# Optimization experiments

Hardware: AMD Instinct MI355X
Metric: run time of the kernel (lower is better)

The kernel has to match this reference:

```python
import jax, jax.numpy as jnp
import numpy as np

B, S, E, H = 4, 2048, 1024, 16
D = E // H  # head dim = 64

def setup_inputs() -> dict:
    key = jax.random.key(0)
    k1, k2, k3 = jax.random.split(key, 3)
    scale = 0.02
    return {
        "x": jax.random.normal(k1, (B, S, E), dtype=jnp.float32),
        "W_qkv": jax.random.normal(k2, (E, 3 * E), dtype=jnp.float32) * scale,
        "b_qkv": jnp.zeros((3 * E,), dtype=jnp.float32),
        "W_o": jax.random.normal(k3, (E, E), dtype=jnp.float32) * scale,
        "b_o": jnp.zeros((E,), dtype=jnp.float32),
    }

def reference(x, W_qkv, b_qkv, W_o, b_o):
    # dropout is identity in eval mode
    qkv = x @ W_qkv + b_qkv                      # [B, S, 3E]
    q, k, v = jnp.split(qkv, 3, axis=-1)          # each [B, S, E]
    def split_heads(t):
        return t.reshape(B, S, H, D).transpose(0, 2, 1, 3)  # [B, H, S, D]
    q, k, v = split_heads(q), split_heads(k), split_heads(v)
    scores = jnp.einsum("bhsd,bhtd->bhst", q, k) / jnp.sqrt(jnp.float32(D))
    causal = jnp.tril(jnp.ones((S, S), dtype=bool))
    scores = jnp.where(causal[None, None], scores, jnp.float32(-jnp.inf))
    attn = jax.nn.softmax(scores, axis=-1)        # [B, H, S, S]
    out = jnp.einsum("bhst,bhtd->bhsd", attn, v)  # [B, H, S, D]
    out = out.transpose(0, 2, 1, 3).reshape(B, S, E)
    return out @ W_o + b_o
```

## Files before the change

### kernel.cpp

```cpp
#include <hip/hip_runtime.h>
#include <stdint.h>

typedef __bf16 bf16_t;
typedef __bf16 bf16x8 __attribute__((ext_vector_type(8)));
typedef float f32x4 __attribute__((ext_vector_type(4)));

#define LOG2E 1.44269504088896340736f

__device__ __forceinline__ float fexp2(float x) {
#if __has_builtin(__builtin_amdgcn_exp2f)
    return __builtin_amdgcn_exp2f(x);
#else
    return exp2f(x);
#endif
}

__device__ __forceinline__ void gld_lds16(const bf16_t* g, bf16_t* l) {
    __builtin_amdgcn_global_load_lds(
        (__attribute__((address_space(1))) void*)(bf16_t*)g,
        (__attribute__((address_space(3))) void*)l,
        16, 0, 0);
}

__global__ __launch_bounds__(256) void prep_k(
    const float* __restrict__ x, bf16_t* __restrict__ xb,
    const float* __restrict__ Wqkv, bf16_t* __restrict__ wqkvT,
    const float* __restrict__ Wo, bf16_t* __restrict__ woT)
{
    __shared__ float t[32][33];
    const int tid = threadIdx.x;
    int blk = blockIdx.x;
    if (blk < 8192) {
        int i = blk * 1024 + tid * 4;
        float4 v = *(const float4*)(x + i);
        union { bf16_t b[4]; uint2 u; } u;
        u.b[0] = (bf16_t)v.x; u.b[1] = (bf16_t)v.y; u.b[2] = (bf16_t)v.z; u.b[3] = (bf16_t)v.w;
        *(uint2*)(xb + i) = u.u;
        return;
    }
    const float* in; bf16_t* out; int C, bx, by;
    if (blk < 11264) { blk -= 8192; in = Wqkv; out = wqkvT; C = 3072; bx = blk % 96; by = blk / 96; }
    else             { blk -= 11264; in = Wo;   out = woT;   C = 1024; bx = blk % 32; by = blk / 32; }
    const int R = 1024;
    const int tx = tid & 31, ty = tid >> 5;
    const int c0 = bx * 32, r0 = by * 32;
    #pragma unroll
    for (int j = 0; j < 32; j += 8)
        t[ty + j][tx] = in[(size_t)(r0 + ty + j) * C + c0 + tx];
    __syncthreads();
    #pragma unroll
    for (int j = 0; j < 32; j += 8)
        out[(size_t)(c0 + ty + j) * R + r0 + tx] = (bf16_t)t[tx][ty + j];
}

__device__ __forceinline__ void gemm_body_pipe(
    const bf16_t* __restrict__ A, const bf16_t* __restrict__ Bt,
    bf16_t* Al, bf16_t* Bl, f32x4 (&acc)[4][4], int m0, int n0)
{
    const int tid = threadIdx.x;
    const int w = tid >> 6, lane = tid & 63;
    const int l15 = lane & 15, quad = lane >> 4;
    const int wm = w >> 2, wn = w & 3;

    const int srow = lane >> 3;
    const int scg = ((lane & 7) ^ srow) * 8;
    const bf16_t* Ag = A  + (size_t)(m0 + w * 16 + srow) * 1024 + scg;
    const bf16_t* Bg = Bt + (size_t)(n0 + w * 32 + srow) * 1024 + scg;

    const int rc0 = (quad ^ (l15 & 7)) * 8;
    const int rc1 = ((quad + 4) ^ (l15 & 7)) * 8;

    auto stage0 = [&](int kt, int ss) {
        gld_lds16(Ag + kt * 64,                       Al + ss * 8192  + (w * 16) * 64);
        gld_lds16(Ag + kt * 64 + (size_t)8 * 1024,    Al + ss * 8192  + (w * 16 + 8) * 64);
        gld_lds16(Bg + kt * 64,                       Bl + ss * 16384 + (w * 32) * 64);
    };
    auto stage1 = [&](int kt, int ss) {
        gld_lds16(Bg + kt * 64 + (size_t)8 * 1024,    Bl + ss * 16384 + (w * 32 + 8) * 64);
        gld_lds16(Bg + kt * 64 + (size_t)16 * 1024,   Bl + ss * 16384 + (w * 32 + 16) * 64);
        gld_lds16(Bg + kt * 64 + (size_t)24 * 1024,   Bl + ss * 16384 + (w * 32 + 24) * 64);
    };

    stage0(0, 0); stage1(0, 0);
    stage0(1, 1); stage1(1, 1);
    asm volatile("s_waitcnt vmcnt(6)" ::: "memory");
    __builtin_amdgcn_s_barrier();

    int cs = 0, ss = 2;
    for (int t = 0; t < 16; ++t) {
        const bf16_t* Ab = Al + cs * 8192;
        const bf16_t* Bb = Bl + cs * 16384;

        {
            bf16x8 af[4], bfr[4];
            #pragma unroll
            for (int mi = 0; mi < 4; mi++)
                af[mi] = *(const bf16x8*)(Ab + (wm * 64 + mi * 16 + l15) * 64 + rc0);
            #pragma unroll
            for (int ni = 0; ni < 4; ni++)
                bfr[ni] = *(const bf16x8*)(Bb + (wn * 64 + ni * 16 + l15) * 64 + rc0);
            if (t < 14) stage0(t + 2, ss);
            __builtin_amdgcn_s_barrier();
            __builtin_amdgcn_s_setprio(1);
            #pragma unroll
            for (int mi = 0; mi < 4; mi++)
                #pragma unroll
                for (int ni = 0; ni < 4; ni++)
                    acc[mi][ni] = __builtin_amdgcn_mfma_f32_16x16x32_bf16(
                        af[mi], bfr[ni], acc[mi][ni], 0, 0, 0);
            __builtin_amdgcn_s_setprio(0);
            __builtin_amdgcn_s_barrier();
        }

        {
            bf16x8 af[4], bfr[4];
            #pragma unroll
            for (int mi = 0; mi < 4; mi++)
                af[mi] = *(const bf16x8*)(Ab + (wm * 64 + mi * 16 + l15) * 64 + rc1);
            #pragma unroll
            for (int ni = 0; ni < 4; ni++)
                bfr[ni] = *(const bf16x8*)(Bb + (wn * 64 + ni * 16 + l15) * 64 + rc1);
            if (t < 14) {
                stage1(t + 2, ss);
                asm volatile("s_waitcnt vmcnt(6)" ::: "memory");
            } else if (t == 14) {
                asm volatile("s_waitcnt vmcnt(0)" ::: "memory");
            }
            __builtin_amdgcn_s_barrier();
            __builtin_amdgcn_s_setprio(1);
            #pragma unroll
            for (int mi = 0; mi < 4; mi++)
                #pragma unroll
                for (int ni = 0; ni < 4; ni++)
                    acc[mi][ni] = __builtin_amdgcn_mfma_f32_16x16x32_bf16(
                        af[mi], bfr[ni], acc[mi][ni], 0, 0, 0);
            __builtin_amdgcn_s_setprio(0);
            __builtin_amdgcn_s_barrier();
        }

        cs = (cs == 2) ? 0 : cs + 1;
        ss = (ss == 2) ? 0 : ss + 1;
    }
}

__global__ __launch_bounds__(512) void gemm_qkv_k(
    const bf16_t* __restrict__ X, const bf16_t* __restrict__ WT,
    const float* __restrict__ bias,
    bf16_t* __restrict__ Qb, bf16_t* __restrict__ Kb, bf16_t* __restrict__ VTb)
{
    __shared__ bf16_t Al[3 * 128 * 64];
    __shared__ bf16_t Bl[3 * 256 * 64];
    const int tid = threadIdx.x;
    const int lane = tid & 63, w = tid >> 6;
    const int l15 = lane & 15, quad = lane >> 4;
    const int wm = w >> 2, wn = w & 3;
    const int n0 = blockIdx.x * 256;
    const int m0 = blockIdx.y * 128;

    f32x4 acc[4][4];
    #pragma unroll
    for (int mi = 0; mi < 4; mi++)
        #pragma unroll
        for (int ni = 0; ni < 4; ni++) acc[mi][ni] = (f32x4){0.f, 0.f, 0.f, 0.f};

    gemm_body_pipe(WT, X, Al, Bl, acc, m0, n0);

    const float QSCALE = 0.125f * LOG2E;
    const int region = m0 >> 10;
    #pragma unroll
    for (int mi = 0; mi < 4; mi++) {
        const int mbase = m0 + wm * 64 + mi * 16 + quad * 4;
        const float4 bia = *(const float4*)(bias + mbase);
        const float ba[4] = {bia.x, bia.y, bia.z, bia.w};
        const int col = mbase & 1023;
        const int h = col >> 6, dbase = col & 63;
        #pragma unroll
        for (int ni = 0; ni < 4; ni++) {
            const int n = n0 + wn * 64 + ni * 16 + l15;
            const int b = n >> 11, s = n & 2047;
            if (region == 0) {
                union { bf16_t bv[4]; uint2 u; } u;
                #pragma unroll
                for (int r = 0; r < 4; r++)
                    u.bv[r] = (bf16_t)((acc[mi][ni][r] + ba[r]) * QSCALE);
                *(uint2*)(Qb + (((size_t)b * 16 + h) * 2048 + s) * 64 + dbase) = u.u;
            } else if (region == 1) {
                union { bf16_t bv[4]; uint2 u; } u;
                #pragma unroll
                for (int r = 0; r < 4; r++)
                    u.bv[r] = (bf16_t)(acc[mi][ni][r] + ba[r]);
                *(uint2*)(Kb + (((size_t)b * 16 + h) * 2048 + s) * 64 + dbase) = u.u;
            } else {
                bf16_t* dst = VTb + (((size_t)b * 16 + h) * 64 + dbase) * 2048 + s;
                #pragma unroll
                for (int r = 0; r < 4; r++)
                    dst[(size_t)r * 2048] = (bf16_t)(acc[mi][ni][r] + ba[r]);
            }
        }
    }
}

__global__ __launch_bounds__(256) void attn_k(
    const bf16_t* __restrict__ Qb, const bf16_t* __restrict__ Kb,
    const bf16_t* __restrict__ VTb, bf16_t* __restrict__ Ob)
{
    __shared__ bf16_t Kl[64 * 64];
    __shared__ bf16_t Vl[64 * 64];
    __shared__ bf16_t Pl[4][16 * 72];

    const int tid = threadIdx.x;
    const int w = tid >> 6, lane = tid & 63;
    const int l15 = lane & 15, quad = lane >> 4;
    const int idx = blockIdx.x;
    const int qt = 31 - (idx >> 6);
    const int bh = idx & 63;
    const int b = bh >> 4, h = bh & 15;
    const int q0 = qt * 64;

    const bf16_t* Qp = Qb + (size_t)bh * 2048 * 64;
    const bf16_t* Kp = Kb + (size_t)bh * 2048 * 64;
    const bf16_t* Vp = VTb + (size_t)bh * 64 * 2048;

    const int srow = w * 16 + (lane >> 3);
    const int scol = ((lane & 7) ^ ((lane >> 3) & 7)) * 8;
    const int rc0 = (quad ^ (l15 & 7)) * 8;
    const int rc1 = ((quad + 4) ^ (l15 & 7)) * 8;

    const int qrow = q0 + w * 16 + l15;
    bf16x8 aq0 = *(const bf16x8*)(Qp + (size_t)qrow * 64 + quad * 8);
    bf16x8 aq1 = *(const bf16x8*)(Qp + (size_t)qrow * 64 + 32 + quad * 8);

    bf16x8 vone;
    #pragma unroll
    for (int j = 0; j < 8; j++) vone[j] = (bf16_t)1.0f;

    f32x4 o[4];
    #pragma unroll
    for (int ni = 0; ni < 4; ni++) o[ni] = (f32x4){0.f, 0.f, 0.f, 0.f};
    f32x4 lacc = (f32x4){0.f, 0.f, 0.f, 0.f};
    const int qloc = w * 16 + l15;

    for (int kv0 = 0; kv0 <= q0; kv0 += 64) {
        __syncthreads();
        gld_lds16(Kp + (size_t)(kv0 + srow) * 64 + scol, Kl + (w * 16) * 64);
        gld_lds16(Kp + (size_t)(kv0 + srow + 8) * 64 + scol, Kl + (w * 16 + 8) * 64);
        gld_lds16(Vp + (size_t)srow * 2048 + kv0 + scol, Vl + (w * 16) * 64);
        gld_lds16(Vp + (size_t)(srow + 8) * 2048 + kv0 + scol, Vl + (w * 16 + 8) * 64);
        __syncthreads();

        f32x4 sv[4];
        #pragma unroll
        for (int ni = 0; ni < 4; ni++) {
            bf16x8 ak0 = *(const bf16x8*)(Kl + (ni * 16 + l15) * 64 + rc0);
            bf16x8 ak1 = *(const bf16x8*)(Kl + (ni * 16 + l15) * 64 + rc1);
            f32x4 z = (f32x4){0.f, 0.f, 0.f, 0.f};
            z = __builtin_amdgcn_mfma_f32_16x16x32_bf16(ak0, aq0, z, 0, 0, 0);
            z = __builtin_amdgcn_mfma_f32_16x16x32_bf16(ak1, aq1, z, 0, 0, 0);
            sv[ni] = z;
        }

        if (kv0 == q0) {
            #pragma unroll
            for (int ni = 0; ni < 4; ni++)
                #pragma unroll
                for (int r = 0; r < 4; r++)
                    if (ni * 16 + quad * 4 + r > qloc) sv[ni][r] = -INFINITY;
        }

        #pragma unroll
        for (int ni = 0; ni < 4; ni++) {
            union { bf16_t bv[4]; uint2 u; } pk;
            #pragma unroll
            for (int r = 0; r < 4; r++) pk.bv[r] = (bf16_t)fexp2(sv[ni][r]);
            *(uint2*)(&Pl[w][l15 * 72 + ni * 16 + quad * 4]) = pk.u;
        }

        bf16x8 pa0 = *(const bf16x8*)(&Pl[w][l15 * 72 + quad * 8]);
        bf16x8 pa1 = *(const bf16x8*)(&Pl[w][l15 * 72 + 32 + quad * 8]);
        #pragma unroll
        for (int ni = 0; ni < 4; ni++) {
            bf16x8 bv0 = *(const bf16x8*)(Vl + (ni * 16 + l15) * 64 + rc0);
            bf16x8 bv1 = *(const bf16x8*)(Vl + (ni * 16 + l15) * 64 + rc1);
            o[ni] = __builtin_amdgcn_mfma_f32_16x16x32_bf16(bv0, pa0, o[ni], 0, 0, 0);
            o[ni] = __builtin_amdgcn_mfma_f32_16x16x32_bf16(bv1, pa1, o[ni], 0, 0, 0);
        }
        lacc = __builtin_amdgcn_mfma_f32_16x16x32_bf16(vone, pa0, lacc, 0, 0, 0);
        lacc = __builtin_amdgcn_mfma_f32_16x16x32_bf16(vone, pa1, lacc, 0, 0, 0);
    }

    const float inv = 1.0f / lacc[0];
    const int s = q0 + w * 16 + l15;
    bf16_t* obase = Ob + ((size_t)b * 2048 + s) * 1024 + h * 64;
    #pragma unroll
    for (int ni = 0; ni < 4; ni++) {
        union { bf16_t bv[4]; uint2 u; } u;
        #pragma unroll
        for (int r = 0; r < 4; r++) u.bv[r] = (bf16_t)(o[ni][r] * inv);
        *(uint2*)(obase + ni * 16 + quad * 4) = u.u;
    }
}

__global__ __launch_bounds__(512) void gemm_out_k(
    const bf16_t* __restrict__ O, const bf16_t* __restrict__ WT,
    const float* __restrict__ bias, float* __restrict__ out)
{
    __shared__ bf16_t Al[3 * 128 * 64];
    __shared__ bf16_t Bl[3 * 256 * 64];
    const int tid = threadIdx.x;
    const int lane = tid & 63, w = tid >> 6;
    const int l15 = lane & 15, quad = lane >> 4;
    const int wm = w >> 2, wn = w & 3;
    const int n0 = blockIdx.x * 256;
    const int m0 = blockIdx.y * 128;

    f32x4 acc[4][4];
    #pragma unroll
    for (int mi = 0; mi < 4; mi++)
        #pragma unroll
        for (int ni = 0; ni < 4; ni++) acc[mi][ni] = (f32x4){0.f, 0.f, 0.f, 0.f};

    gemm_body_pipe(WT, O, Al, Bl, acc, m0, n0);

    #pragma unroll
    for (int mi = 0; mi < 4; mi++) {
        const int mbase = m0 + wm * 64 + mi * 16 + quad * 4;
        const float4 bia = *(const float4*)(bias + mbase);
        #pragma unroll
        for (int ni = 0; ni < 4; ni++) {
            const int n = n0 + wn * 64 + ni * 16 + l15;
            float4 v;
            v.x = acc[mi][ni][0] + bia.x;
            v.y = acc[mi][ni][1] + bia.y;
            v.z = acc[mi][ni][2] + bia.z;
            v.w = acc[mi][ni][3] + bia.w;
            *(float4*)(out + (size_t)n * 1024 + mbase) = v;
        }
    }
}


extern "C" void kernel_launch(void* const* d_in, const int* in_sizes, int n_in,
                              void* d_out, int out_size, void* d_ws, size_t ws_size,
                              hipStream_t stream) {
    const float* x     = (const float*)d_in[0];
    const float* W_qkv = (const float*)d_in[1];
    const float* b_qkv = (const float*)d_in[2];
    const float* W_o   = (const float*)d_in[3];
    const float* b_o   = (const float*)d_in[4];
    float* out = (float*)d_out;

    char* ws = (char*)d_ws;
    size_t off = 0;
    auto alloc = [&](size_t bytes) -> void* {
        void* p = ws + off;
        off += (bytes + 255) & ~(size_t)255;
        return p;
    };
    bf16_t* xb    = (bf16_t*)alloc((size_t)8192 * 1024 * 2);
    bf16_t* wqkvT = (bf16_t*)alloc((size_t)3072 * 1024 * 2);
    bf16_t* woT   = (bf16_t*)alloc((size_t)1024 * 1024 * 2);
    bf16_t* Qb    = (bf16_t*)alloc((size_t)8192 * 1024 * 2);
    bf16_t* Kb    = (bf16_t*)alloc((size_t)8192 * 1024 * 2);
    bf16_t* VTb   = (bf16_t*)alloc((size_t)8192 * 1024 * 2);
    bf16_t* Ob    = xb;

    prep_k<<<12288, 256, 0, stream>>>(x, xb, W_qkv, wqkvT, W_o, woT);
    gemm_qkv_k<<<dim3(32, 24), 512, 0, stream>>>(xb, wqkvT, b_qkv, Qb, Kb, VTb);
    attn_k<<<2048, 256, 0, stream>>>(Qb, Kb, VTb, Ob);
    gemm_out_k<<<dim3(32, 8), 512, 0, stream>>>(Ob, woT, b_o, out);
}
```

Baseline: 237.4 us.

## Rewrite QKV GEMM with 256x256 tiles and double-buffered four-phase MFMA schedule

The QKV projection GEMM now uses a standalone kernel with a 256x256 block tile (8 warps each computing 128x64), double-buffered LDS and a four-phase interleave of fragment loads, async global-to-LDS staging and MFMA bursts. The grid is halved to 32x12. The goal is more operand reuse per LDS byte and fewer blocks. The costs are more accumulator registers (launch bounds of 512 threads with 2 blocks per CU), a full vmcnt(0) wait each iteration instead of a deeper three-stage pipeline, and fewer blocks to fill the CUs. The attention kernel is moved in the file but its code is unchanged.

```diff
diff --git a/kernel.cpp b/kernel.cpp
--- a/kernel.cpp
+++ b/kernel.cpp
@@ -53,6 +53,271 @@
         out[(size_t)(c0 + ty + j) * R + r0 + tx] = (bf16_t)t[tx][ty + j];
 }
 
+__global__ __launch_bounds__(512, 2) void gemm_qkv_k(
+    const bf16_t* __restrict__ X, const bf16_t* __restrict__ WT,
+    const float* __restrict__ bias,
+    bf16_t* __restrict__ Qb, bf16_t* __restrict__ Kb, bf16_t* __restrict__ VTb)
+{
+    __shared__ bf16_t Al[2 * 256 * 64];
+    __shared__ bf16_t Bl[2 * 256 * 64];
+    const int tid = threadIdx.x;
+    const int lane = tid & 63, w = tid >> 6;
+    const int l15 = lane & 15, quad = lane >> 4;
+    const int wr = w >> 2, wc = w & 3;
+    const int n0 = blockIdx.x * 256;
+    const int m0 = blockIdx.y * 256;
+
+    const int srow = lane >> 3;
+    const int scg = ((lane & 7) ^ srow) * 8;
+    const bf16_t* Ag = WT + (size_t)(m0 + w * 32 + srow) * 1024 + scg;
+    const bf16_t* Bg = X  + (size_t)(n0 + w * 32 + srow) * 1024 + scg;
+
+    const int rc0 = (quad ^ (l15 & 7)) * 8;
+    const int rc1 = ((quad + 4) ^ (l15 & 7)) * 8;
+
+    f32x4 acc[8][4];
+    #pragma unroll
+    for (int mi = 0; mi < 8; mi++)
+        #pragma unroll
+        for (int ni = 0; ni < 4; ni++) acc[mi][ni] = (f32x4){0.f, 0.f, 0.f, 0.f};
+
+    auto stageA = [&](int kt, int t) {
+        #pragma unroll
+        for (int j = 0; j < 4; j++)
+            gld_lds16(Ag + (size_t)kt * 64 + (size_t)(j * 8) * 1024,
+                      Al + t * 16384 + (w * 32 + j * 8) * 64);
+    };
+    auto stageB = [&](int kt, int t) {
+        #pragma unroll
+        for (int j = 0; j < 4; j++)
+            gld_lds16(Bg + (size_t)kt * 64 + (size_t)(j * 8) * 1024,
+                      Bl + t * 16384 + (w * 32 + j * 8) * 64);
+    };
+
+    stageA(0, 0); stageB(0, 0);
+    asm volatile("s_waitcnt vmcnt(0)" ::: "memory");
+    __builtin_amdgcn_s_barrier();
+
+    int cs = 0;
+    #pragma unroll 1
+    for (int n = 0; n < 16; ++n) {
+        const bf16_t* Ab = Al + cs * 16384;
+        const bf16_t* Bb = Bl + cs * 16384;
+        bf16x8 afr[4][2], bfr[4][2];
+
+        #pragma unroll
+        for (int q = 0; q < 4; q++) {
+            afr[q][0] = *(const bf16x8*)(Ab + (wr * 128 + q * 16 + l15) * 64 + rc0);
+            afr[q][1] = *(const bf16x8*)(Ab + (wr * 128 + q * 16 + l15) * 64 + rc1);
+        }
+        #pragma unroll
+        for (int ni = 0; ni < 2; ni++) {
+            bfr[ni][0] = *(const bf16x8*)(Bb + (wc * 64 + ni * 16 + l15) * 64 + rc0);
+            bfr[ni][1] = *(const bf16x8*)(Bb + (wc * 64 + ni * 16 + l15) * 64 + rc1);
+        }
+        if (n < 15) stageA(n + 1, cs ^ 1);
+        __builtin_amdgcn_s_barrier();
+        __builtin_amdgcn_s_setprio(1);
+        #pragma unroll
+        for (int q = 0; q < 4; q++)
+            #pragma unroll
+            for (int ni = 0; ni < 2; ni++) {
+                acc[q][ni] = __builtin_amdgcn_mfma_f32_16x16x32_bf16(
+                    afr[q][0], bfr[ni][0], acc[q][ni], 0, 0, 0);
+                acc[q][ni] = __builtin_amdgcn_mfma_f32_16x16x32_bf16(
+                    afr[q][1], bfr[ni][1], acc[q][ni], 0, 0, 0);
+            }
+        __builtin_amdgcn_s_setprio(0);
+
+        #pragma unroll
+        for (int ni = 2; ni < 4; ni++) {
+            bfr[ni][0] = *(const bf16x8*)(Bb + (wc * 64 + ni * 16 + l15) * 64 + rc0);
+            bfr[ni][1] = *(const bf16x8*)(Bb + (wc * 64 + ni * 16 + l15) * 64 + rc1);
+        }
+        if (n < 15) stageB(n + 1, cs ^ 1);
+        __builtin_amdgcn_s_barrier();
+        __builtin_amdgcn_s_setprio(1);
+        #pragma unroll
+        for (int q = 0; q < 4; q++)
+            #pragma unroll
+            for (int ni = 2; ni < 4; ni++) {
+                acc[q][ni] = __builtin_amdgcn_mfma_f32_16x16x32_bf16(
+                    afr[q][0], bfr[ni][0], acc[q][ni], 0, 0, 0);
+                acc[q][ni] = __builtin_amdgcn_mfma_f32_16x16x32_bf16(
+                    afr[q][1], bfr[ni][1], acc[q][ni], 0, 0, 0);
+            }
+        __builtin_amdgcn_s_setprio(0);
+
+        #pragma unroll
+        for (int q = 0; q < 4; q++) {
+            afr[q][0] = *(const bf16x8*)(Ab + (wr * 128 + 64 + q * 16 + l15) * 64 + rc0);
+            afr[q][1] = *(const bf16x8*)(Ab + (wr * 128 + 64 + q * 16 + l15) * 64 + rc1);
+        }
+        __builtin_amdgcn_s_barrier();
+        __builtin_amdgcn_s_setprio(1);
+        #pragma unroll
+        for (int q = 0; q < 4; q++)
+            #pragma unroll
+            for (int ni = 2; ni < 4; ni++) {
+                acc[4 + q][ni] = __builtin_amdgcn_mfma_f32_16x16x32_bf16(
+                    afr[q][0], bfr[ni][0], acc[4 + q][ni], 0, 0, 0);
+                acc[4 + q][ni] = __builtin_amdgcn_mfma_f32_16x16x32_bf16(
+                    afr[q][1], bfr[ni][1], acc[4 + q][ni], 0, 0, 0);
+            }
+        __builtin_amdgcn_s_setprio(0);
+
+        asm volatile("s_waitcnt vmcnt(0)" ::: "memory");
+        __builtin_amdgcn_s_barrier();
+        __builtin_amdgcn_s_setprio(1);
+        #pragma unroll
+        for (int q = 0; q < 4; q++)
+            #pragma unroll
+            for (int ni = 0; ni < 2; ni++) {
+                acc[4 + q][ni] = __builtin_amdgcn_mfma_f32_16x16x32_bf16(
+                    afr[q][0], bfr[ni][0], acc[4 + q][ni], 0, 0, 0);
+                acc[4 + q][ni] = __builtin_amdgcn_mfma_f32_16x16x32_bf16(
+                    afr[q][1], bfr[ni][1], acc[4 + q][ni], 0, 0, 0);
+            }
+        __builtin_amdgcn_s_setprio(0);
+
+        cs ^= 1;
+    }
+
+    const float QSCALE = 0.125f * LOG2E;
+    const int region = m0 >> 10;
+    #pragma unroll
+    for (int mi = 0; mi < 8; mi++) {
+        const int mbase = m0 + wr * 128 + mi * 16 + quad * 4;
+        const float4 bia = *(const float4*)(bias + mbase);
+        const float ba[4] = {bia.x, bia.y, bia.z, bia.w};
+        const int col = mbase & 1023;
+        const int h = col >> 6, dbase = col & 63;
+        #pragma unroll
+        for (int ni = 0; ni < 4; ni++) {
+            const int n = n0 + wc * 64 + ni * 16 + l15;
+            const int b = n >> 11, s = n & 2047;
+            if (region == 0) {
+                union { bf16_t bv[4]; uint2 u; } u;
+                #pragma unroll
+                for (int r = 0; r < 4; r++)
+                    u.bv[r] = (bf16_t)((acc[mi][ni][r] + ba[r]) * QSCALE);
+                *(uint2*)(Qb + (((size_t)b * 16 + h) * 2048 + s) * 64 + dbase) = u.u;
+            } else if (region == 1) {
+                union { bf16_t bv[4]; uint2 u; } u;
+                #pragma unroll
+                for (int r = 0; r < 4; r++)
+                    u.bv[r] = (bf16_t)(acc[mi][ni][r] + ba[r]);
+                *(uint2*)(Kb + (((size_t)b * 16 + h) * 2048 + s) * 64 + dbase) = u.u;
+            } else {
+                bf16_t* dst = VTb + (((size_t)b * 16 + h) * 64 + dbase) * 2048 + s;
+                #pragma unroll
+                for (int r = 0; r < 4; r++)
+                    dst[(size_t)r * 2048] = (bf16_t)(acc[mi][ni][r] + ba[r]);
+            }
+        }
+    }
+}
+
+__global__ __launch_bounds__(256) void attn_k(
+    const bf16_t* __restrict__ Qb, const bf16_t* __restrict__ Kb,
+    const bf16_t* __restrict__ VTb, bf16_t* __restrict__ Ob)
+{
+    __shared__ bf16_t Kl[64 * 64];
+    __shared__ bf16_t Vl[64 * 64];
+    __shared__ bf16_t Pl[4][16 * 72];
+
+    const int tid = threadIdx.x;
+    const int w = tid >> 6, lane = tid & 63;
+    const int l15 = lane & 15, quad = lane >> 4;
+    const int idx = blockIdx.x;
+    const int qt = 31 - (idx >> 6);
+    const int bh = idx & 63;
+    const int b = bh >> 4, h = bh & 15;
+    const int q0 = qt * 64;
+
+    const bf16_t* Qp = Qb + (size_t)bh * 2048 * 64;
+    const bf16_t* Kp = Kb + (size_t)bh * 2048 * 64;
+    const bf16_t* Vp = VTb + (size_t)bh * 64 * 2048;
+
+    const int srow = w * 16 + (lane >> 3);
+    const int scol = ((lane & 7) ^ ((lane >> 3) & 7)) * 8;
+    const int rc0 = (quad ^ (l15 & 7)) * 8;
+    const int rc1 = ((quad + 4) ^ (l15 & 7)) * 8;
+
+    const int qrow = q0 + w * 16 + l15;
+    bf16x8 aq0 = *(const bf16x8*)(Qp + (size_t)qrow * 64 + quad * 8);
+    bf16x8 aq1 = *(const bf16x8*)(Qp + (size_t)qrow * 64 + 32 + quad * 8);
+
+    bf16x8 vone;
+    #pragma unroll
+    for (int j = 0; j < 8; j++) vone[j] = (bf16_t)1.0f;
+
+    f32x4 o[4];
+    #pragma unroll
+    for (int ni = 0; ni < 4; ni++) o[ni] = (f32x4){0.f, 0.f, 0.f, 0.f};
+    f32x4 lacc = (f32x4){0.f, 0.f, 0.f, 0.f};
+    const int qloc = w * 16 + l15;
+
+    for (int kv0 = 0; kv0 <= q0; kv0 += 64) {
+        __syncthreads();
+        gld_lds16(Kp + (size_t)(kv0 + srow) * 64 + scol, Kl + (w * 16) * 64);
+        gld_lds16(Kp + (size_t)(kv0 + srow + 8) * 64 + scol, Kl + (w * 16 + 8) * 64);
+        gld_lds16(Vp + (size_t)srow * 2048 + kv0 + scol, Vl + (w * 16) * 64);
+        gld_lds16(Vp + (size_t)(srow + 8) * 2048 + kv0 + scol, Vl + (w * 16 + 8) * 64);
+        __syncthreads();
+
+        f32x4 sv[4];
+        #pragma unroll
+        for (int ni = 0; ni < 4; ni++) {
+            bf16x8 ak0 = *(const bf16x8*)(Kl + (ni * 16 + l15) * 64 + rc0);
+            bf16x8 ak1 = *(const bf16x8*)(Kl + (ni * 16 + l15) * 64 + rc1);
+            f32x4 z = (f32x4){0.f, 0.f, 0.f, 0.f};
+            z = __builtin_amdgcn_mfma_f32_16x16x32_bf16(ak0, aq0, z, 0, 0, 0);
+            z = __builtin_amdgcn_mfma_f32_16x16x32_bf16(ak1, aq1, z, 0, 0, 0);
+            sv[ni] = z;
+        }
+
+        if (kv0 == q0) {
+            #pragma unroll
+            for (int ni = 0; ni < 4; ni++)
+                #pragma unroll
+                for (int r = 0; r < 4; r++)
+                    if (ni * 16 + quad * 4 + r > qloc) sv[ni][r] = -INFINITY;
+        }
+
+        #pragma unroll
+        for (int ni = 0; ni < 4; ni++) {
+            union { bf16_t bv[4]; uint2 u; } pk;
+            #pragma unroll
+            for (int r = 0; r < 4; r++) pk.bv[r] = (bf16_t)fexp2(sv[ni][r]);
+            *(uint2*)(&Pl[w][l15 * 72 + ni * 16 + quad * 4]) = pk.u;
+        }
+
+        bf16x8 pa0 = *(const bf16x8*)(&Pl[w][l15 * 72 + quad * 8]);
+        bf16x8 pa1 = *(const bf16x8*)(&Pl[w][l15 * 72 + 32 + quad * 8]);
+        #pragma unroll
+        for (int ni = 0; ni < 4; ni++) {
+            bf16x8 bv0 = *(const bf16x8*)(Vl + (ni * 16 + l15) * 64 + rc0);
+            bf16x8 bv1 = *(const bf16x8*)(Vl + (ni * 16 + l15) * 64 + rc1);
+            o[ni] = __builtin_amdgcn_mfma_f32_16x16x32_bf16(bv0, pa0, o[ni], 0, 0, 0);
+            o[ni] = __builtin_amdgcn_mfma_f32_16x16x32_bf16(bv1, pa1, o[ni], 0, 0, 0);
+        }
+        lacc = __builtin_amdgcn_mfma_f32_16x16x32_bf16(vone, pa0, lacc, 0, 0, 0);
+        lacc = __builtin_amdgcn_mfma_f32_16x16x32_bf16(vone, pa1, lacc, 0, 0, 0);
+    }
+
+    const float inv = 1.0f / lacc[0];
+    const int s = q0 + w * 16 + l15;
+    bf16_t* obase = Ob + ((size_t)b * 2048 + s) * 1024 + h * 64;
+    #pragma unroll
+    for (int ni = 0; ni < 4; ni++) {
+        union { bf16_t bv[4]; uint2 u; } u;
+        #pragma unroll
+        for (int r = 0; r < 4; r++) u.bv[r] = (bf16_t)(o[ni][r] * inv);
+        *(uint2*)(obase + ni * 16 + quad * 4) = u.u;
+    }
+}
+
 __device__ __forceinline__ void gemm_body_pipe(
     const bf16_t* __restrict__ A, const bf16_t* __restrict__ Bt,
     bf16_t* Al, bf16_t* Bl, f32x4 (&acc)[4][4], int m0, int n0)
@@ -90,7 +355,6 @@
     for (int t = 0; t < 16; ++t) {
         const bf16_t* Ab = Al + cs * 8192;
         const bf16_t* Bb = Bl + cs * 16384;
-
         {
             bf16x8 af[4], bfr[4];
             #pragma unroll
@@ -111,7 +375,6 @@
             __builtin_amdgcn_s_setprio(0);
             __builtin_amdgcn_s_barrier();
         }
-
         {
             bf16x8 af[4], bfr[4];
             #pragma unroll
@@ -137,166 +400,8 @@
             __builtin_amdgcn_s_setprio(0);
             __builtin_amdgcn_s_barrier();
         }
-
         cs = (cs == 2) ? 0 : cs + 1;
         ss = (ss == 2) ? 0 : ss + 1;
-    }
-}
-
-__global__ __launch_bounds__(512) void gemm_qkv_k(
-    const bf16_t* __restrict__ X, const bf16_t* __restrict__ WT,
-    const float* __restrict__ bias,
-    bf16_t* __restrict__ Qb, bf16_t* __restrict__ Kb, bf16_t* __restrict__ VTb)
-{
-    __shared__ bf16_t Al[3 * 128 * 64];
-    __shared__ bf16_t Bl[3 * 256 * 64];
-    const int tid = threadIdx.x;
-    const int lane = tid & 63, w = tid >> 6;
-    const int l15 = lane & 15, quad = lane >> 4;
-    const int wm = w >> 2, wn = w & 3;
-    const int n0 = blockIdx.x * 256;
-    const int m0 = blockIdx.y * 128;
-
-    f32x4 acc[4][4];
-    #pragma unroll
-    for (int mi = 0; mi < 4; mi++)
-        #pragma unroll
-        for (int ni = 0; ni < 4; ni++) acc[mi][ni] = (f32x4){0.f, 0.f, 0.f, 0.f};
-
-    gemm_body_pipe(WT, X, Al, Bl, acc, m0, n0);
-
-    const float QSCALE = 0.125f * LOG2E;
-    const int region = m0 >> 10;
-    #pragma unroll
-    for (int mi = 0; mi < 4; mi++) {
-        const int mbase = m0 + wm * 64 + mi * 16 + quad * 4;
-        const float4 bia = *(const float4*)(bias + mbase);
-        const float ba[4] = {bia.x, bia.y, bia.z, bia.w};
-        const int col = mbase & 1023;
-        const int h = col >> 6, dbase = col & 63;
-        #pragma unroll
-        for (int ni = 0; ni < 4; ni++) {
-            const int n = n0 + wn * 64 + ni * 16 + l15;
-            const int b = n >> 11, s = n & 2047;
-            if (region == 0) {
-                union { bf16_t bv[4]; uint2 u; } u;
-                #pragma unroll
-                for (int r = 0; r < 4; r++)
-                    u.bv[r] = (bf16_t)((acc[mi][ni][r] + ba[r]) * QSCALE);
-                *(uint2*)(Qb + (((size_t)b * 16 + h) * 2048 + s) * 64 + dbase) = u.u;
-            } else if (region == 1) {
-                union { bf16_t bv[4]; uint2 u; } u;
-                #pragma unroll
-                for (int r = 0; r < 4; r++)
-                    u.bv[r] = (bf16_t)(acc[mi][ni][r] + ba[r]);
-                *(uint2*)(Kb + (((size_t)b * 16 + h) * 2048 + s) * 64 + dbase) = u.u;
-            } else {
-                bf16_t* dst = VTb + (((size_t)b * 16 + h) * 64 + dbase) * 2048 + s;
-                #pragma unroll
-                for (int r = 0; r < 4; r++)
-                    dst[(size_t)r * 2048] = (bf16_t)(acc[mi][ni][r] + ba[r]);
-            }
-        }
-    }
-}
-
-__global__ __launch_bounds__(256) void attn_k(
-    const bf16_t* __restrict__ Qb, const bf16_t* __restrict__ Kb,
-    const bf16_t* __restrict__ VTb, bf16_t* __restrict__ Ob)
-{
-    __shared__ bf16_t Kl[64 * 64];
-    __shared__ bf16_t Vl[64 * 64];
-    __shared__ bf16_t Pl[4][16 * 72];
-
-    const int tid = threadIdx.x;
-    const int w = tid >> 6, lane = tid & 63;
-    const int l15 = lane & 15, quad = lane >> 4;
-    const int idx = blockIdx.x;
-    const int qt = 31 - (idx >> 6);
-    const int bh = idx & 63;
-    const int b = bh >> 4, h = bh & 15;
-    const int q0 = qt * 64;
-
-    const bf16_t* Qp = Qb + (size_t)bh * 2048 * 64;
-    const bf16_t* Kp = Kb + (size_t)bh * 2048 * 64;
-    const bf16_t* Vp = VTb + (size_t)bh * 64 * 2048;
-
-    const int srow = w * 16 + (lane >> 3);
-    const int scol = ((lane & 7) ^ ((lane >> 3) & 7)) * 8;
-    const int rc0 = (quad ^ (l15 & 7)) * 8;
-    const int rc1 = ((quad + 4) ^ (l15 & 7)) * 8;
-
-    const int qrow = q0 + w * 16 + l15;
-    bf16x8 aq0 = *(const bf16x8*)(Qp + (size_t)qrow * 64 + quad * 8);
-    bf16x8 aq1 = *(const bf16x8*)(Qp + (size_t)qrow * 64 + 32 + quad * 8);
-
-    bf16x8 vone;
-    #pragma unroll
-    for (int j = 0; j < 8; j++) vone[j] = (bf16_t)1.0f;
-
-    f32x4 o[4];
-    #pragma unroll
-    for (int ni = 0; ni < 4; ni++) o[ni] = (f32x4){0.f, 0.f, 0.f, 0.f};
-    f32x4 lacc = (f32x4){0.f, 0.f, 0.f, 0.f};
-    const int qloc = w * 16 + l15;
-
-    for (int kv0 = 0; kv0 <= q0; kv0 += 64) {
-        __syncthreads();
-        gld_lds16(Kp + (size_t)(kv0 + srow) * 64 + scol, Kl + (w * 16) * 64);
-        gld_lds16(Kp + (size_t)(kv0 + srow + 8) * 64 + scol, Kl + (w * 16 + 8) * 64);
-        gld_lds16(Vp + (size_t)srow * 2048 + kv0 + scol, Vl + (w * 16) * 64);
-        gld_lds16(Vp + (size_t)(srow + 8) * 2048 + kv0 + scol, Vl + (w * 16 + 8) * 64);
-        __syncthreads();
-
-        f32x4 sv[4];
-        #pragma unroll
-        for (int ni = 0; ni < 4; ni++) {
-            bf16x8 ak0 = *(const bf16x8*)(Kl + (ni * 16 + l15) * 64 + rc0);
-            bf16x8 ak1 = *(const bf16x8*)(Kl + (ni * 16 + l15) * 64 + rc1);
-            f32x4 z = (f32x4){0.f, 0.f, 0.f, 0.f};
-            z = __builtin_amdgcn_mfma_f32_16x16x32_bf16(ak0, aq0, z, 0, 0, 0);
-            z = __builtin_amdgcn_mfma_f32_16x16x32_bf16(ak1, aq1, z, 0, 0, 0);
-            sv[ni] = z;
-        }
-
-        if (kv0 == q0) {
-            #pragma unroll
-            for (int ni = 0; ni < 4; ni++)
-                #pragma unroll
-                for (int r = 0; r < 4; r++)
-                    if (ni * 16 + quad * 4 + r > qloc) sv[ni][r] = -INFINITY;
-        }
-
-        #pragma unroll
-        for (int ni = 0; ni < 4; ni++) {
-            union { bf16_t bv[4]; uint2 u; } pk;
-            #pragma unroll
-            for (int r = 0; r < 4; r++) pk.bv[r] = (bf16_t)fexp2(sv[ni][r]);
-            *(uint2*)(&Pl[w][l15 * 72 + ni * 16 + quad * 4]) = pk.u;
-        }
-
-        bf16x8 pa0 = *(const bf16x8*)(&Pl[w][l15 * 72 + quad * 8]);
-        bf16x8 pa1 = *(const bf16x8*)(&Pl[w][l15 * 72 + 32 + quad * 8]);
-        #pragma unroll
-        for (int ni = 0; ni < 4; ni++) {
-            bf16x8 bv0 = *(const bf16x8*)(Vl + (ni * 16 + l15) * 64 + rc0);
-            bf16x8 bv1 = *(const bf16x8*)(Vl + (ni * 16 + l15) * 64 + rc1);
-            o[ni] = __builtin_amdgcn_mfma_f32_16x16x32_bf16(bv0, pa0, o[ni], 0, 0, 0);
-            o[ni] = __builtin_amdgcn_mfma_f32_16x16x32_bf16(bv1, pa1, o[ni], 0, 0, 0);
-        }
-        lacc = __builtin_amdgcn_mfma_f32_16x16x32_bf16(vone, pa0, lacc, 0, 0, 0);
-        lacc = __builtin_amdgcn_mfma_f32_16x16x32_bf16(vone, pa1, lacc, 0, 0, 0);
-    }
-
-    const float inv = 1.0f / lacc[0];
-    const int s = q0 + w * 16 + l15;
-    bf16_t* obase = Ob + ((size_t)b * 2048 + s) * 1024 + h * 64;
-    #pragma unroll
-    for (int ni = 0; ni < 4; ni++) {
-        union { bf16_t bv[4]; uint2 u; } u;
-        #pragma unroll
-        for (int r = 0; r < 4; r++) u.bv[r] = (bf16_t)(o[ni][r] * inv);
-        *(uint2*)(obase + ni * 16 + quad * 4) = u.u;
     }
 }
 
@@ -365,7 +470,7 @@
     bf16_t* Ob    = xb;
 
     prep_k<<<12288, 256, 0, stream>>>(x, xb, W_qkv, wqkvT, W_o, woT);
-    gemm_qkv_k<<<dim3(32, 24), 512, 0, stream>>>(xb, wqkvT, b_qkv, Qb, Kb, VTb);
+    gemm_qkv_k<<<dim3(32, 12), 512, 0, stream>>>(xb, wqkvT, b_qkv, Qb, Kb, VTb);
     attn_k<<<2048, 256, 0, stream>>>(Qb, Kb, VTb, Ob);
     gemm_out_k<<<dim3(32, 8), 512, 0, stream>>>(Ob, woT, b_o, out);
 }
```

After: 246.0 us. 3.6% more time.

## Process 128 query rows per attention block to reuse K/V tiles

Applied to the files above, without the earlier changes.

Each attention block now covers 128 query rows, with each warp handling two 16-row groups, so every K/V tile staged in LDS feeds twice as many queries. K and V fragments are loaded into registers once per tile and reused for both groups. The grid is halved, which reduces parallelism and causal load balance. The last two diagonal tiles are processed by all warps even where fully masked, which adds some wasted work.

```diff
diff --git a/kernel.cpp b/kernel.cpp
--- a/kernel.cpp
+++ b/kernel.cpp
@@ -90,7 +90,6 @@
     for (int t = 0; t < 16; ++t) {
         const bf16_t* Ab = Al + cs * 8192;
         const bf16_t* Bb = Bl + cs * 16384;
-
         {
             bf16x8 af[4], bfr[4];
             #pragma unroll
@@ -111,7 +110,6 @@
             __builtin_amdgcn_s_setprio(0);
             __builtin_amdgcn_s_barrier();
         }
-
         {
             bf16x8 af[4], bfr[4];
             #pragma unroll
@@ -137,7 +135,6 @@
             __builtin_amdgcn_s_setprio(0);
             __builtin_amdgcn_s_barrier();
         }
-
         cs = (cs == 2) ? 0 : cs + 1;
         ss = (ss == 2) ? 0 : ss + 1;
     }
@@ -206,16 +203,16 @@
 {
     __shared__ bf16_t Kl[64 * 64];
     __shared__ bf16_t Vl[64 * 64];
-    __shared__ bf16_t Pl[4][16 * 72];
+    __shared__ bf16_t Pl[4][32 * 72];
 
     const int tid = threadIdx.x;
     const int w = tid >> 6, lane = tid & 63;
     const int l15 = lane & 15, quad = lane >> 4;
     const int idx = blockIdx.x;
-    const int qt = 31 - (idx >> 6);
+    const int qt = 15 - (idx >> 6);
     const int bh = idx & 63;
     const int b = bh >> 4, h = bh & 15;
-    const int q0 = qt * 64;
+    const int q0 = qt * 128;
 
     const bf16_t* Qp = Qb + (size_t)bh * 2048 * 64;
     const bf16_t* Kp = Kb + (size_t)bh * 2048 * 64;
@@ -226,21 +223,28 @@
     const int rc0 = (quad ^ (l15 & 7)) * 8;
     const int rc1 = ((quad + 4) ^ (l15 & 7)) * 8;
 
-    const int qrow = q0 + w * 16 + l15;
-    bf16x8 aq0 = *(const bf16x8*)(Qp + (size_t)qrow * 64 + quad * 8);
-    bf16x8 aq1 = *(const bf16x8*)(Qp + (size_t)qrow * 64 + 32 + quad * 8);
+    bf16x8 aq[2][2];
+    #pragma unroll
+    for (int g = 0; g < 2; g++) {
+        const int qrow = q0 + w * 32 + g * 16 + l15;
+        aq[g][0] = *(const bf16x8*)(Qp + (size_t)qrow * 64 + quad * 8);
+        aq[g][1] = *(const bf16x8*)(Qp + (size_t)qrow * 64 + 32 + quad * 8);
+    }
 
     bf16x8 vone;
     #pragma unroll
     for (int j = 0; j < 8; j++) vone[j] = (bf16_t)1.0f;
 
-    f32x4 o[4];
-    #pragma unroll
-    for (int ni = 0; ni < 4; ni++) o[ni] = (f32x4){0.f, 0.f, 0.f, 0.f};
-    f32x4 lacc = (f32x4){0.f, 0.f, 0.f, 0.f};
-    const int qloc = w * 16 + l15;
-
-    for (int kv0 = 0; kv0 <= q0; kv0 += 64) {
+    f32x4 o[2][4];
+    #pragma unroll
+    for (int g = 0; g < 2; g++)
+        #pragma unroll
+        for (int ni = 0; ni < 4; ni++) o[g][ni] = (f32x4){0.f, 0.f, 0.f, 0.f};
+    f32x4 lacc[2];
+    lacc[0] = (f32x4){0.f, 0.f, 0.f, 0.f};
+    lacc[1] = (f32x4){0.f, 0.f, 0.f, 0.f};
+
+    for (int kv0 = 0; kv0 <= q0 + 64; kv0 += 64) {
         __syncthreads();
         gld_lds16(Kp + (size_t)(kv0 + srow) * 64 + scol, Kl + (w * 16) * 64);
         gld_lds16(Kp + (size_t)(kv0 + srow + 8) * 64 + scol, Kl + (w * 16 + 8) * 64);
@@ -248,55 +252,71 @@
         gld_lds16(Vp + (size_t)(srow + 8) * 2048 + kv0 + scol, Vl + (w * 16 + 8) * 64);
         __syncthreads();
 
-        f32x4 sv[4];
-        #pragma unroll
-        for (int ni = 0; ni < 4; ni++) {
-            bf16x8 ak0 = *(const bf16x8*)(Kl + (ni * 16 + l15) * 64 + rc0);
-            bf16x8 ak1 = *(const bf16x8*)(Kl + (ni * 16 + l15) * 64 + rc1);
-            f32x4 z = (f32x4){0.f, 0.f, 0.f, 0.f};
-            z = __builtin_amdgcn_mfma_f32_16x16x32_bf16(ak0, aq0, z, 0, 0, 0);
-            z = __builtin_amdgcn_mfma_f32_16x16x32_bf16(ak1, aq1, z, 0, 0, 0);
-            sv[ni] = z;
-        }
-
-        if (kv0 == q0) {
-            #pragma unroll
-            for (int ni = 0; ni < 4; ni++)
-                #pragma unroll
-                for (int r = 0; r < 4; r++)
-                    if (ni * 16 + quad * 4 + r > qloc) sv[ni][r] = -INFINITY;
-        }
-
-        #pragma unroll
-        for (int ni = 0; ni < 4; ni++) {
-            union { bf16_t bv[4]; uint2 u; } pk;
-            #pragma unroll
-            for (int r = 0; r < 4; r++) pk.bv[r] = (bf16_t)fexp2(sv[ni][r]);
-            *(uint2*)(&Pl[w][l15 * 72 + ni * 16 + quad * 4]) = pk.u;
-        }
-
-        bf16x8 pa0 = *(const bf16x8*)(&Pl[w][l15 * 72 + quad * 8]);
-        bf16x8 pa1 = *(const bf16x8*)(&Pl[w][l15 * 72 + 32 + quad * 8]);
-        #pragma unroll
-        for (int ni = 0; ni < 4; ni++) {
-            bf16x8 bv0 = *(const bf16x8*)(Vl + (ni * 16 + l15) * 64 + rc0);
-            bf16x8 bv1 = *(const bf16x8*)(Vl + (ni * 16 + l15) * 64 + rc1);
-            o[ni] = __builtin_amdgcn_mfma_f32_16x16x32_bf16(bv0, pa0, o[ni], 0, 0, 0);
-            o[ni] = __builtin_amdgcn_mfma_f32_16x16x32_bf16(bv1, pa1, o[ni], 0, 0, 0);
-        }
-        lacc = __builtin_amdgcn_mfma_f32_16x16x32_bf16(vone, pa0, lacc, 0, 0, 0);
-        lacc = __builtin_amdgcn_mfma_f32_16x16x32_bf16(vone, pa1, lacc, 0, 0, 0);
-    }
-
-    const float inv = 1.0f / lacc[0];
-    const int s = q0 + w * 16 + l15;
-    bf16_t* obase = Ob + ((size_t)b * 2048 + s) * 1024 + h * 64;
-    #pragma unroll
-    for (int ni = 0; ni < 4; ni++) {
-        union { bf16_t bv[4]; uint2 u; } u;
-        #pragma unroll
-        for (int r = 0; r < 4; r++) u.bv[r] = (bf16_t)(o[ni][r] * inv);
-        *(uint2*)(obase + ni * 16 + quad * 4) = u.u;
+        bf16x8 ak[4][2], bv[4][2];
+        #pragma unroll
+        for (int ni = 0; ni < 4; ni++) {
+            ak[ni][0] = *(const bf16x8*)(Kl + (ni * 16 + l15) * 64 + rc0);
+            ak[ni][1] = *(const bf16x8*)(Kl + (ni * 16 + l15) * 64 + rc1);
+        }
+        #pragma unroll
+        for (int ni = 0; ni < 4; ni++) {
+            bv[ni][0] = *(const bf16x8*)(Vl + (ni * 16 + l15) * 64 + rc0);
+            bv[ni][1] = *(const bf16x8*)(Vl + (ni * 16 + l15) * 64 + rc1);
+        }
+
+        #pragma unroll
+        for (int g = 0; g < 2; g++) {
+            const int qloc = w * 32 + g * 16 + l15;
+            f32x4 sv[4];
+            #pragma unroll
+            for (int ni = 0; ni < 4; ni++) {
+                f32x4 z = (f32x4){0.f, 0.f, 0.f, 0.f};
+                z = __builtin_amdgcn_mfma_f32_16x16x32_bf16(ak[ni][0], aq[g][0], z, 0, 0, 0);
+                z = __builtin_amdgcn_mfma_f32_16x16x32_bf16(ak[ni][1], aq[g][1], z, 0, 0, 0);
+                sv[ni] = z;
+            }
+
+            if (kv0 >= q0) {
+                const int koff = kv0 - q0;
+                #pragma unroll
+                for (int ni = 0; ni < 4; ni++)
+                    #pragma unroll
+                    for (int r = 0; r < 4; r++)
+                        if (koff + ni * 16 + quad * 4 + r > qloc) sv[ni][r] = -INFINITY;
+            }
+
+            #pragma unroll
+            for (int ni = 0; ni < 4; ni++) {
+                union { bf16_t bvv[4]; uint2 u; } pk;
+                #pragma unroll
+                for (int r = 0; r < 4; r++) pk.bvv[r] = (bf16_t)fexp2(sv[ni][r]);
+                *(uint2*)(&Pl[w][(g * 16 + l15) * 72 + ni * 16 + quad * 4]) = pk.u;
+            }
+
+            bf16x8 pa0 = *(const bf16x8*)(&Pl[w][(g * 16 + l15) * 72 + quad * 8]);
+            bf16x8 pa1 = *(const bf16x8*)(&Pl[w][(g * 16 + l15) * 72 + 32 + quad * 8]);
+            #pragma unroll
+            for (int ni = 0; ni < 4; ni++) {
+                o[g][ni] = __builtin_amdgcn_mfma_f32_16x16x32_bf16(bv[ni][0], pa0, o[g][ni], 0, 0, 0);
+                o[g][ni] = __builtin_amdgcn_mfma_f32_16x16x32_bf16(bv[ni][1], pa1, o[g][ni], 0, 0, 0);
+            }
+            lacc[g] = __builtin_amdgcn_mfma_f32_16x16x32_bf16(vone, pa0, lacc[g], 0, 0, 0);
+            lacc[g] = __builtin_amdgcn_mfma_f32_16x16x32_bf16(vone, pa1, lacc[g], 0, 0, 0);
+        }
+    }
+
+    #pragma unroll
+    for (int g = 0; g < 2; g++) {
+        const float inv = 1.0f / lacc[g][0];
+        const int s = q0 + w * 32 + g * 16 + l15;
+        bf16_t* obase = Ob + ((size_t)b * 2048 + s) * 1024 + h * 64;
+        #pragma unroll
+        for (int ni = 0; ni < 4; ni++) {
+            union { bf16_t bvv[4]; uint2 u; } u;
+            #pragma unroll
+            for (int r = 0; r < 4; r++) u.bvv[r] = (bf16_t)(o[g][ni][r] * inv);
+            *(uint2*)(obase + ni * 16 + quad * 4) = u.u;
+        }
     }
 }
 
@@ -366,6 +386,6 @@
 
     prep_k<<<12288, 256, 0, stream>>>(x, xb, W_qkv, wqkvT, W_o, woT);
     gemm_qkv_k<<<dim3(32, 24), 512, 0, stream>>>(xb, wqkvT, b_qkv, Qb, Kb, VTb);
-    attn_k<<<2048, 256, 0, stream>>>(Qb, Kb, VTb, Ob);
+    attn_k<<<1024, 256, 0, stream>>>(Qb, Kb, VTb, Ob);
     gemm_out_k<<<dim3(32, 8), 512, 0, stream>>>(Ob, woT, b_o, out);
 }
```

After: 244.5 us. 3.0% more time.
